# Kernel tuning notes

Measured on AMD Instinct MI355X. Metric: run time of the kernel, lower is better.

Reference implementation:

```python
import jax, jax.numpy as jnp
import numpy as np

B, N, E = 64, 512, 8192          # graphs, nodes per graph, edges per graph
F_IN, H, C = 128, 128, 10        # in features, hidden, classes
K1, K2 = 256, 128                # dense pool cluster counts: ceil(.5*N), ceil(.5*K1)
EPS = 1e-15


def setup_inputs():
    key = jax.random.key(0)
    keys = jax.random.split(key, 32)
    it = iter(keys)
    def w(shape, fan_in):
        return jax.random.normal(next(it), shape, jnp.float32) / np.sqrt(fan_in)
    x = jax.random.normal(next(it), (B * N, F_IN), jnp.float32)
    src_l = jax.random.randint(next(it), (B, E), 0, N)
    dst_l = jax.random.randint(next(it), (B, E), 0, N)
    off = (jnp.arange(B) * N)[:, None]
    src = (src_l + off).reshape(-1).astype(jnp.int32)
    dst = (dst_l + off).reshape(-1).astype(jnp.int32)
    return dict(
        x=x, src=src, dst=dst,
        conv0_wr=w((F_IN, H), F_IN), conv0_wroot=w((F_IN, H), F_IN), conv0_b=jnp.zeros((H,), jnp.float32),
        sconv2_wr=w((H, H), H), sconv2_wroot=w((H, H), H), sconv2_b=jnp.zeros((H,), jnp.float32),
        sconv3_wr=w((H, H), H), sconv3_wroot=w((H, H), H), sconv3_b=jnp.zeros((H,), jnp.float32),
        sage1_wr=w((H, H), H), sage1_wroot=w((H, H), H), sage1_b=jnp.zeros((H,), jnp.float32),
        sage2_wr=w((H, H), H), sage2_wroot=w((H, H), H), sage2_b=jnp.zeros((H,), jnp.float32),
        pool0_w=w((H, K1), H), pool0_b=jnp.zeros((K1,), jnp.float32),
        pool1_w=w((H, K2), H), pool1_b=jnp.zeros((K2,), jnp.float32),
        p1=w((H,), H), p2=w((H,), H), p3=w((H,), H),
        lin1_1_w=w((2 * H, H), 2 * H), lin1_1_b=jnp.zeros((H,), jnp.float32),
        lin1_w=w((H, H), H), lin1_b=jnp.zeros((H,), jnp.float32),
        lin2_w=w((2 * H, C), 2 * H), lin2_b=jnp.zeros((C,), jnp.float32),
    )


def _graph_conv(x, src, dst, emask, wr, wroot, b, n):
    # PyG GraphConv: lin_rel(sum_j x_j) + lin_root(x_i); invalid edges masked to 0.
    msg = x[src] * emask[:, None]
    agg = jax.ops.segment_sum(msg, dst, num_segments=n)
    return agg @ wr + x @ wroot + b


def _topk_pool(x, score_w, src, dst, emask, n_per_graph, k):
    # TopK pooling (MPoolS): score = x.w/||w||, keep top ratio*n per graph, gate by tanh(score).
    score = x @ score_w / (jnp.linalg.norm(score_w) + 1e-16)
    idx = jax.lax.top_k(score.reshape(B, n_per_graph), k)[1]
    perm = (idx + (jnp.arange(B) * n_per_graph)[:, None]).reshape(-1)
    new_x = x[perm] * jnp.tanh(score[perm])[:, None]
    new_id = jnp.full((B * n_per_graph,), -1, jnp.int32).at[perm].set(
        jnp.arange(B * k, dtype=jnp.int32))
    ns, nd = new_id[src], new_id[dst]
    valid = (ns >= 0) & (nd >= 0) & (emask > 0)
    return new_x, jnp.where(valid, ns, 0), jnp.where(valid, nd, 0), valid.astype(x.dtype)


def _readout(x, k):
    # gmp || gap per graph (nodes are contiguous, k per graph)
    xr = x.reshape(B, k, -1)
    return jnp.concatenate([xr.max(axis=1), xr.mean(axis=1)], axis=-1)


def _dense_sage(x, adj, wr, wroot, b):
    agg = (adj @ x) / jnp.clip(adj.sum(-1, keepdims=True), 1.0, None)
    return agg @ wr + x @ wroot + b


def _dense_mincut_pool(x, adj, s):
    s = jax.nn.softmax(s, axis=-1)
    k = s.shape[-1]
    out = jnp.einsum('bnk,bnf->bkf', s, x)
    out_adj = jnp.einsum('bnk,bnm,bml->bkl', s, adj, s)
    mincut_num = jnp.trace(out_adj, axis1=-2, axis2=-1)
    deg = adj.sum(-1)
    mincut_den = jnp.einsum('bn,bnk,bnk->b', deg, s, s)
    mc = -jnp.mean(mincut_num / (mincut_den + EPS))
    ss = jnp.einsum('bnk,bnl->bkl', s, s)
    ss_n = jnp.linalg.norm(ss, axis=(1, 2), keepdims=True)
    eye = jnp.eye(k, dtype=x.dtype)
    o = jnp.mean(jnp.linalg.norm(ss / (ss_n + EPS) - eye / jnp.sqrt(k), axis=(1, 2)))
    di = jnp.arange(k)
    out_adj = out_adj.at[:, di, di].set(0.0)
    dpool = jnp.sqrt(out_adj.sum(-1)) + EPS
    out_adj = out_adj / dpool[:, :, None] / dpool[:, None, :]
    return out, out_adj, mc, o


def _forward(x, src, dst, conv0_wr, conv0_wroot, conv0_b, sconv2_wr, sconv2_wroot, sconv2_b,
             sconv3_wr, sconv3_wroot, sconv3_b, sage1_wr, sage1_wroot, sage1_b,
             sage2_wr, sage2_wroot, sage2_b, pool0_w, pool0_b, pool1_w, pool1_b,
             p1, p2, p3, lin1_1_w, lin1_1_b, lin1_w, lin1_b, lin2_w, lin2_b):
    relu = jax.nn.relu
    e0 = jnp.ones((src.shape[0],), x.dtype)
    x0 = relu(_graph_conv(x, src, dst, e0, conv0_wr, conv0_wroot, conv0_b, B * N))
    # ---- sparse (MPoolS / top-k) branch, stage 1 ----
    sx, s1, d1, m1 = _topk_pool(x0, p1, src, dst, e0, N, N // 2)
    sx1 = _readout(sx, N // 2)
    # ---- dense (DiffPool-style) branch ----
    xd = x0.reshape(B, N, H)                               # to_dense_batch (full mask)
    g = src // N
    adj = jnp.zeros((B, N, N), x.dtype).at[g, src % N, dst % N].add(1.0)  # to_dense_adj
    s = xd @ pool0_w + pool0_b
    xd, adj, mc, o = _dense_mincut_pool(xd, adj, s)
    xd = relu(_dense_sage(xd, adj, sage1_wr, sage1_wroot, sage1_b))
    s = xd @ pool1_w + pool1_b
    xd, adj, mc2, o2 = _dense_mincut_pool(xd, adj, s)
    mc, o = mc + mc2, o + o2
    xd = _dense_sage(xd, adj, sage2_wr, sage2_wroot, sage2_b)
    xg = relu(xd.mean(axis=1) @ lin1_w + lin1_b)
    # ---- sparse branch, stages 2 and 3 ----
    sx = relu(_graph_conv(sx, s1, d1, m1, sconv2_wr, sconv2_wroot, sconv2_b, B * (N // 2)))
    sx, s2, d2, m2 = _topk_pool(sx, p2, s1, d1, m1, N // 2, N // 4)
    sx2 = _readout(sx, N // 4)
    sx = relu(_graph_conv(sx, s2, d2, m2, sconv3_wr, sconv3_wroot, sconv3_b, B * (N // 4)))
    sx, s3, d3, m3 = _topk_pool(sx, p3, s2, d2, m2, N // 4, N // 8)
    sx3 = _readout(sx, N // 8)
    sxr = relu((sx1 + sx2 + sx3) @ lin1_1_w + lin1_1_b)
    logits = jnp.concatenate([sxr, xg], axis=-1) @ lin2_w + lin2_b
    return logits, mc, o


def reference(x, src, dst, conv0_wr, conv0_wroot, conv0_b, sconv2_wr, sconv2_wroot, sconv2_b,
              sconv3_wr, sconv3_wroot, sconv3_b, sage1_wr, sage1_wroot, sage1_b,
              sage2_wr, sage2_wroot, sage2_b, pool0_w, pool0_b, pool1_w, pool1_b,
              p1, p2, p3, lin1_1_w, lin1_1_b, lin1_w, lin1_b, lin2_w, lin2_b):
    return _forward(x, src, dst, conv0_wr, conv0_wroot, conv0_b, sconv2_wr, sconv2_wroot,
                    sconv2_b, sconv3_wr, sconv3_wroot, sconv3_b, sage1_wr, sage1_wroot,
                    sage1_b, sage2_wr, sage2_wroot, sage2_b, pool0_w, pool0_b, pool1_w,
                    pool1_b, p1, p2, p3, lin1_1_w, lin1_1_b, lin1_w, lin1_b, lin2_w, lin2_b)
```

## Files before the change

### kernel.cpp

```cpp
#include <hip/hip_runtime.h>
#include <math.h>

#define NGRAPH 64
#define NE 524288
#define EPG 8192
#define TSZ 2560

typedef short s16x8 __attribute__((ext_vector_type(8)));
typedef float f32x4 __attribute__((ext_vector_type(4)));

__device__ inline unsigned short f2bf(float f) {
    unsigned int u = __float_as_uint(f);
    return (unsigned short)((u + 0x7FFFu + ((u >> 16) & 1u)) >> 16);
}
__device__ inline float bf2f(unsigned short h) {
    return __uint_as_float((unsigned int)h << 16);
}
__device__ inline unsigned int f2pk(float v) {
    unsigned short h = f2bf(v);
    return (unsigned int)h | ((unsigned int)f2bf(v - bf2f(h)) << 16);
}

__global__ void edge_count2(const int* __restrict__ keyA, int* __restrict__ cntA,
                            const int* __restrict__ keyB, int* __restrict__ cntB) {
    int e = blockIdx.x * 256 + threadIdx.x;
    if (e >= NE) return;
    if (blockIdx.y == 0) atomicAdd(&cntA[keyA[e]], 1);
    else                 atomicAdd(&cntB[keyB[e]], 1);
}

__device__ inline void scan_body(const int* __restrict__ counts, int* __restrict__ offs,
                                 int* __restrict__ cursor, int nPerGraph,
                                 float* __restrict__ degOut, int* s) {
    const int g = blockIdx.x, t = threadIdx.x;
    int v = (t < nPerGraph) ? counts[g * nPerGraph + t] : 0;
    s[t] = v; __syncthreads();
    for (int d = 1; d < 512; d <<= 1) {
        int u = (t >= d) ? s[t - d] : 0;
        __syncthreads();
        s[t] += u;
        __syncthreads();
    }
    if (t < nPerGraph) {
        int o = g * EPG + s[t] - v;
        offs[g * nPerGraph + t] = o;
        cursor[g * nPerGraph + t] = o;
        if (degOut) degOut[g * nPerGraph + t] = (float)v;
    }
}

__global__ __launch_bounds__(512) void scan_offsets(const int* __restrict__ counts,
        int* __restrict__ offs, int* __restrict__ cursor, int nPerGraph,
        float* __restrict__ degOut) {
    __shared__ int s[512];
    scan_body(counts, offs, cursor, nPerGraph, degOut, s);
}

__global__ __launch_bounds__(512) void scan_offsets2(
        const int* __restrict__ cA, int* __restrict__ oA, int* __restrict__ uA,
        const int* __restrict__ cB, int* __restrict__ oB, int* __restrict__ uB,
        int nPerGraph, float* __restrict__ degB) {
    __shared__ int s[512];
    if (blockIdx.y == 0) scan_body(cA, oA, uA, nPerGraph, nullptr, s);
    else                 scan_body(cB, oB, uB, nPerGraph, degB, s);
}

__global__ void edge_fill(const int* __restrict__ key, const int* __restrict__ payload,
                          const float* __restrict__ mask, int* __restrict__ cursor,
                          int* __restrict__ elist) {
    int e = blockIdx.x * 256 + threadIdx.x;
    if (e < NE && (!mask || mask[e] > 0.f)) {
        int p = atomicAdd(&cursor[key[e]], 1);
        elist[p] = payload[e];
    }
}

__global__ void edge_fill2(const int* __restrict__ kA, const int* __restrict__ pA,
                           int* __restrict__ uA, int* __restrict__ eA,
                           const int* __restrict__ kB, const int* __restrict__ pB,
                           int* __restrict__ uB, int* __restrict__ eB) {
    int e = blockIdx.x * 256 + threadIdx.x;
    if (e >= NE) return;
    if (blockIdx.y == 0) { int p = atomicAdd(&uA[kA[e]], 1); eA[p] = pA[e]; }
    else                 { int p = atomicAdd(&uB[kB[e]], 1); eB[p] = pB[e]; }
}

__global__ __launch_bounds__(256) void gather_csr(
    const float* __restrict__ xfeat, int Fx,
    const int* __restrict__ offs, const int* __restrict__ cnts,
    const int* __restrict__ elist,
    float* __restrict__ out, unsigned int* __restrict__ opk,
    int totRows, int rowsPerGraph)
{
    const int gid = (blockIdx.x * 256 + threadIdx.x) >> 5;
    const int lane = threadIdx.x & 31;
    const int csh = (Fx == 256) ? 1 : 0;
    const int rid = gid >> csh;
    const int c0 = (gid & ((1 << csh) - 1)) << 7;
    if (rid >= totRows) return;
    const int row = (rid & 63) * rowsPerGraph + (rid >> 6);
    const int beg = offs[row];
    const int n = cnts[row];
    const long long co = (long long)c0 + (lane << 2);
    float4 acc = make_float4(0.f, 0.f, 0.f, 0.f);
    int j = 0;
    for (; j + 4 <= n; j += 4) {
        const int n0 = elist[beg + j], n1 = elist[beg + j + 1];
        const int n2 = elist[beg + j + 2], n3 = elist[beg + j + 3];
        const float4 v0 = *(const float4*)&xfeat[(long long)n0 * Fx + co];
        const float4 v1 = *(const float4*)&xfeat[(long long)n1 * Fx + co];
        const float4 v2 = *(const float4*)&xfeat[(long long)n2 * Fx + co];
        const float4 v3 = *(const float4*)&xfeat[(long long)n3 * Fx + co];
        acc.x += v0.x + v1.x + v2.x + v3.x;
        acc.y += v0.y + v1.y + v2.y + v3.y;
        acc.z += v0.z + v1.z + v2.z + v3.z;
        acc.w += v0.w + v1.w + v2.w + v3.w;
    }
    for (; j < n; ++j) {
        const float4 v = *(const float4*)&xfeat[(long long)elist[beg + j] * Fx + co];
        acc.x += v.x; acc.y += v.y; acc.z += v.z; acc.w += v.w;
    }
    if (opk) {
        uint4 pk;
        pk.x = f2pk(acc.x); pk.y = f2pk(acc.y); pk.z = f2pk(acc.z); pk.w = f2pk(acc.w);
        *(uint4*)&opk[(long long)row * Fx + co] = pk;
    } else {
        *(float4*)&out[(long long)row * Fx + co] = acc;
    }
}

struct WSpec {
    const float* w1; const float* w2; int K1; int K2; int Nn;
    unsigned short* oh; unsigned short* ol;
};

__global__ void wconv_all(WSpec s0, WSpec s1, WSpec s2, WSpec s3, WSpec s4, WSpec s5, WSpec s6) {
    WSpec s;
    switch (blockIdx.y) {
        case 0: s = s0; break; case 1: s = s1; break; case 2: s = s2; break;
        case 3: s = s3; break; case 4: s = s4; break; case 5: s = s5; break;
        default: s = s6; break;
    }
    int idx = blockIdx.x * 256 + threadIdx.x;
    int Kt = s.K1 + s.K2;
    if (idx >= s.Nn * Kt) return;
    int n = idx / Kt, k = idx - n * Kt;
    float v = (k < s.K1) ? s.w1[(long long)k * s.Nn + n] : s.w2[(long long)(k - s.K1) * s.Nn + n];
    unsigned short h = f2bf(v);
    s.oh[idx] = h;
    s.ol[idx] = f2bf(v - __uint_as_float((unsigned int)h << 16));
}

__device__ inline void stageN_split(const float* __restrict__ src, int ldk, int k0,
                                    short* lds, int tid, const float* __restrict__ rs, int m0) {
    const int r = tid >> 2, kq = (tid & 3) << 3;
    const float* p = src + (long long)r * ldk + k0 + kq;
    float v[8];
    *(float4*)v = *(const float4*)p;
    *(float4*)(v + 4) = *(const float4*)(p + 4);
    if (rs) { float s = rs[m0 + r]; for (int i = 0; i < 8; ++i) v[i] *= s; }
    s16x8 hv, lv;
    #pragma unroll
    for (int i = 0; i < 8; ++i) {
        unsigned short h = f2bf(v[i]);
        float hf = __uint_as_float((unsigned int)h << 16);
        hv[i] = (short)h;
        lv[i] = (short)f2bf(v[i] - hf);
    }
    *(s16x8*)(lds + r * 40 + kq) = hv;
    *(s16x8*)(lds + TSZ + r * 40 + kq) = lv;
}

__device__ inline void stageT_pk(const unsigned int* __restrict__ P,
                                 int ldm, int k0, int m0, short* lds, int tid) {
    const int kp = tid >> 4, mc = tid & 15;
    const int k = kp << 1;
    const unsigned int* p0 = P + (long long)(k0 + k) * ldm + m0 + mc;
    const unsigned int* p1 = p0 + ldm;
    #pragma unroll
    for (int i = 0; i < 4; ++i) {
        unsigned int e0 = p0[i << 4], e1 = p1[i << 4];
        const int o = (mc + (i << 4)) * 40 + k;
        *(unsigned int*)(lds + o) = (e0 & 0xffffu) | (e1 << 16);
        *(unsigned int*)(lds + o + TSZ) = (e0 >> 16) | (e1 & 0xffff0000u);
    }
}

__device__ inline void stageT_hi_pk(const unsigned int* __restrict__ P,
                                    int ldm, int k0, int m0, short* lds, int tid) {
    const int kp = tid >> 4, mc = tid & 15;
    const int k = kp << 1;
    const unsigned int* p0 = P + (long long)(k0 + k) * ldm + m0 + mc;
    const unsigned int* p1 = p0 + ldm;
    #pragma unroll
    for (int i = 0; i < 4; ++i) {
        unsigned int e0 = p0[i << 4], e1 = p1[i << 4];
        *(unsigned int*)(lds + (mc + (i << 4)) * 40 + k) = (e0 & 0xffffu) | (e1 << 16);
    }
}

__device__ inline void stageW_split(const unsigned short* __restrict__ wh,
                                    const unsigned short* __restrict__ wl, int ldk,
                                    int n0, int k0, short* lds, int tid) {
    const int r = tid >> 2, kq = (tid & 3) << 3;
    *(s16x8*)(lds + r * 40 + kq) = *(const s16x8*)(wh + (long long)(n0 + r) * ldk + k0 + kq);
    *(s16x8*)(lds + TSZ + r * 40 + kq) = *(const s16x8*)(wl + (long long)(n0 + r) * ldk + k0 + kq);
}

__device__ inline void mfma_split(const short* As, const short* Bs, int wm, int wn,
                                  int l15, int quad, f32x4 (&acc)[2][2]) {
    const int ko = quad << 3;
    s16x8 ah[2], al[2], bh[2], bl[2];
    #pragma unroll
    for (int i = 0; i < 2; ++i) {
        const int ra = (wm + (i << 4) + l15) * 40 + ko;
        const int rb = (wn + (i << 4) + l15) * 40 + ko;
        ah[i] = *(const s16x8*)&As[ra];
        al[i] = *(const s16x8*)&As[TSZ + ra];
        bh[i] = *(const s16x8*)&Bs[rb];
        bl[i] = *(const s16x8*)&Bs[TSZ + rb];
    }
    #pragma unroll
    for (int mi = 0; mi < 2; ++mi)
    #pragma unroll
    for (int ni = 0; ni < 2; ++ni) {
        f32x4 c = acc[mi][ni];
        c = __builtin_amdgcn_mfma_f32_16x16x32_bf16(ah[mi], bh[ni], c, 0, 0, 0);
        c = __builtin_amdgcn_mfma_f32_16x16x32_bf16(ah[mi], bl[ni], c, 0, 0, 0);
        c = __builtin_amdgcn_mfma_f32_16x16x32_bf16(al[mi], bh[ni], c, 0, 0, 0);
        acc[mi][ni] = c;
    }
}

__device__ inline void mfma_hi(const short* As, const short* Bs, int wm, int wn,
                               int l15, int quad, f32x4 (&acc)[2][2]) {
    const int ko = quad << 3;
    s16x8 ah[2], bh[2];
    #pragma unroll
    for (int i = 0; i < 2; ++i) {
        ah[i] = *(const s16x8*)&As[(wm + (i << 4) + l15) * 40 + ko];
        bh[i] = *(const s16x8*)&Bs[(wn + (i << 4) + l15) * 40 + ko];
    }
    #pragma unroll
    for (int mi = 0; mi < 2; ++mi)
    #pragma unroll
    for (int ni = 0; ni < 2; ++ni)
        acc[mi][ni] = __builtin_amdgcn_mfma_f32_16x16x32_bf16(ah[mi], bh[ni], acc[mi][ni], 0, 0, 0);
}

__global__ __launch_bounds__(256) void gemm_aw(
    const float* __restrict__ A1, int K1, const float* __restrict__ A2, int K2,
    const float* __restrict__ rscale,
    const unsigned short* __restrict__ Wh, const unsigned short* __restrict__ Wl,
    const float* __restrict__ bias, float* __restrict__ C,
    unsigned int* __restrict__ Cpk,
    int Nn, int doRelu)
{
    __shared__ short As[2 * TSZ], Bs[2 * TSZ];
    const int m0 = blockIdx.y << 6, n0 = blockIdx.x << 6;
    const int tid = threadIdx.x, lane = tid & 63, wv = tid >> 6;
    const int l15 = lane & 15, quad = lane >> 4;
    const int wm = (wv & 1) << 5, wn = (wv >> 1) << 5;
    f32x4 acc[2][2] = {};
    const int Kt = K1 + K2;
    for (int k0 = 0; k0 < Kt; k0 += 32) {
        if (k0 < K1) stageN_split(A1 + (long long)m0 * K1, K1, k0, As, tid, rscale, m0);
        else         stageN_split(A2 + (long long)m0 * K2, K2, k0 - K1, As, tid, nullptr, 0);
        stageW_split(Wh, Wl, Kt, n0, k0, Bs, tid);
        __syncthreads();
        mfma_split(As, Bs, wm, wn, l15, quad, acc);
        __syncthreads();
    }
    #pragma unroll
    for (int mi = 0; mi < 2; ++mi)
    #pragma unroll
    for (int ni = 0; ni < 2; ++ni) {
        const int col = n0 + wn + (ni << 4) + l15;
        const float bv = bias ? bias[col] : 0.f;
        #pragma unroll
        for (int r = 0; r < 4; ++r) {
            const int row = m0 + wm + (mi << 4) + (quad << 2) + r;
            float v = acc[mi][ni][r] + bv;
            if (doRelu) v = fmaxf(v, 0.f);
            C[(long long)row * Nn + col] = v;
            if (Cpk) Cpk[(long long)row * Nn + col] = f2pk(v);
        }
    }
}

__global__ __launch_bounds__(256) void gemm_tt(
    const unsigned int* __restrict__ Ap, const unsigned int* __restrict__ Bp,
    float* __restrict__ C, unsigned int* __restrict__ Cpk,
    float* __restrict__ fro,
    int Kd, int Mm, int Nn, int dual,
    long long sA, long long sB, long long sC)
{
    __shared__ short As[2 * TSZ], Bs[2 * TSZ], A2s[TSZ];
    __shared__ float redf[4];
    const int z = blockIdx.x;
    const unsigned int* Apz = Ap + (long long)z * sA;
    const unsigned int* Bpz = Bp + (long long)z * sB;
    const int m0 = blockIdx.y << 6, n0 = blockIdx.z << 6;
    const int tid = threadIdx.x, lane = tid & 63, wv = tid >> 6;
    const int l15 = lane & 15, quad = lane >> 4;
    const int wm = (wv & 1) << 5, wn = (wv >> 1) << 5;
    const int fw = dual ? ((m0 < n0) ? 2 : ((m0 == n0) ? 1 : 0)) : 0;
    f32x4 acc[2][2] = {};
    f32x4 accA[2][2] = {};
    for (int k0 = 0; k0 < Kd; k0 += 32) {
        stageT_pk(Apz, Mm, k0, m0, As, tid);
        stageT_pk(Bpz, Nn, k0, n0, Bs, tid);
        if (fw) stageT_hi_pk(Apz, Mm, k0, n0, A2s, tid);
        __syncthreads();
        mfma_split(As, Bs, wm, wn, l15, quad, acc);
        if (fw) mfma_hi(As, A2s, wm, wn, l15, quad, accA);
        __syncthreads();
    }
    float* Cp = C ? C + (long long)z * sC : nullptr;
    unsigned int* Ckp = Cpk ? Cpk + (long long)z * sC : nullptr;
    #pragma unroll
    for (int mi = 0; mi < 2; ++mi)
    #pragma unroll
    for (int ni = 0; ni < 2; ++ni) {
        const int col = n0 + wn + (ni << 4) + l15;
        #pragma unroll
        for (int r = 0; r < 4; ++r) {
            const int row = m0 + wm + (mi << 4) + (quad << 2) + r;
            const float v = acc[mi][ni][r];
            if (Cp) Cp[(long long)row * Nn + col] = v;
            if (Ckp) Ckp[(long long)row * Nn + col] = f2pk(v);
        }
    }
    if (fw) {
        float s = 0.f;
        #pragma unroll
        for (int mi = 0; mi < 2; ++mi)
        #pragma unroll
        for (int ni = 0; ni < 2; ++ni)
        #pragma unroll
        for (int r = 0; r < 4; ++r) s += accA[mi][ni][r] * accA[mi][ni][r];
        s *= (float)fw;
        for (int off = 32; off; off >>= 1) s += __shfl_xor(s, off);
        if (lane == 0) redf[wv] = s;
        __syncthreads();
        if (tid == 0) atomicAdd(&fro[z], redf[0] + redf[1] + redf[2] + redf[3]);
    }
}

__global__ __launch_bounds__(256) void gemm_nt(
    const unsigned short* __restrict__ Ah, const unsigned short* __restrict__ Al,
    const unsigned int* __restrict__ Bp,
    float* __restrict__ C, unsigned int* __restrict__ Cpk,
    int Kd, int Nn, long long sA, long long sB, long long sC)
{
    __shared__ short As[2 * TSZ], Bs[2 * TSZ];
    const int z = blockIdx.x;
    const int m0 = blockIdx.y << 6, n0 = blockIdx.z << 6;
    const unsigned short* Aph = Ah + (long long)z * sA;
    const unsigned short* Apl = Al + (long long)z * sA;
    const unsigned int* Bpz = Bp + (long long)z * sB;
    const int tid = threadIdx.x, lane = tid & 63, wv = tid >> 6;
    const int l15 = lane & 15, quad = lane >> 4;
    const int wm = (wv & 1) << 5, wn = (wv >> 1) << 5;
    f32x4 acc[2][2] = {};
    for (int k0 = 0; k0 < Kd; k0 += 32) {
        stageW_split(Aph, Apl, Kd, m0, k0, As, tid);
        stageT_pk(Bpz, Nn, k0, n0, Bs, tid);
        __syncthreads();
        mfma_split(As, Bs, wm, wn, l15, quad, acc);
        __syncthreads();
    }
    #pragma unroll
    for (int mi = 0; mi < 2; ++mi)
    #pragma unroll
    for (int ni = 0; ni < 2; ++ni) {
        const int col = n0 + wn + (ni << 4) + l15;
        #pragma unroll
        for (int r = 0; r < 4; ++r) {
            const int row = m0 + wm + (mi << 4) + (quad << 2) + r;
            const float v = acc[mi][ni][r];
            if (C) C[(long long)z * sC + (long long)row * Nn + col] = v;
            if (Cpk) Cpk[(long long)z * sC + (long long)row * Nn + col] = f2pk(v);
        }
    }
}

__global__ __launch_bounds__(256) void softmax_rows_wave(
    float* __restrict__ sm, int L,
    const float* __restrict__ deg,
    float* __restrict__ rowq2, float* __restrict__ rowdq2, int totRows,
    unsigned int* __restrict__ opk)
{
    const int wid = (blockIdx.x * 256 + threadIdx.x) >> 6;
    const int lane = threadIdx.x & 63;
    if (wid >= totRows) return;
    float* rowp = sm + (long long)wid * L;
    const int nv = L >> 6;
    float v[4];
    if (nv == 4) {
        float4 t = *(const float4*)&rowp[lane << 2];
        v[0] = t.x; v[1] = t.y; v[2] = t.z; v[3] = t.w;
    } else {
        float2 t = *(const float2*)&rowp[lane << 1];
        v[0] = t.x; v[1] = t.y;
    }
    float mx = v[0];
    for (int i = 1; i < nv; ++i) mx = fmaxf(mx, v[i]);
    for (int off = 32; off; off >>= 1) mx = fmaxf(mx, __shfl_xor(mx, off));
    float s = 0.f;
    for (int i = 0; i < nv; ++i) { v[i] = expf(v[i] - mx); s += v[i]; }
    for (int off = 32; off; off >>= 1) s += __shfl_xor(s, off);
    const float inv = 1.f / s;
    float q2 = 0.f;
    for (int i = 0; i < nv; ++i) { float p = v[i] * inv; v[i] = p; q2 += p * p; }
    if (nv == 4) *(float4*)&rowp[lane << 2] = make_float4(v[0], v[1], v[2], v[3]);
    else         *(float2*)&rowp[lane << 1] = make_float2(v[0], v[1]);
    const long long rb = (long long)wid * L;
    if (nv == 4) {
        uint4 pk;
        pk.x = f2pk(v[0]); pk.y = f2pk(v[1]); pk.z = f2pk(v[2]); pk.w = f2pk(v[3]);
        *(uint4*)&opk[rb + (lane << 2)] = pk;
    } else {
        uint2 pk;
        pk.x = f2pk(v[0]); pk.y = f2pk(v[1]);
        *(uint2*)&opk[rb + (lane << 1)] = pk;
    }
    for (int off = 32; off; off >>= 1) q2 += __shfl_xor(q2, off);
    if (lane == 0) { rowq2[wid] = q2; rowdq2[wid] = deg[wid] * q2; }
}

__global__ __launch_bounds__(256) void zdiag_rowsum_wave(
    float* __restrict__ adj, int K, float* __restrict__ dpool,
    float* __restrict__ rowdiag, int totRows)
{
    const int wid = (blockIdx.x * 256 + threadIdx.x) >> 6;
    const int lane = threadIdx.x & 63;
    if (wid >= totRows) return;
    const int b = wid / K;
    const int dcol = wid - b * K;
    float* rowp = adj + (long long)wid * K;
    const int nv = K >> 6;
    float s = 0.f, dval = 0.f;
    for (int q = 0; q < nv; ++q) {
        int c = lane + (q << 6);
        float v = rowp[c];
        if (c == dcol) { dval = v; rowp[c] = 0.f; v = 0.f; }
        s += v;
    }
    for (int off = 32; off; off >>= 1) s += __shfl_xor(s, off);
    if (lane == (dcol & 63)) rowdiag[wid] = dval;
    if (lane == 0) dpool[wid] = sqrtf(s) + 1e-15f;
}

__global__ __launch_bounds__(256) void norm_adj_wave(
    const float* __restrict__ adj, int K, const float* __restrict__ dpool,
    float* __restrict__ rowsum, float* __restrict__ rscale,
    unsigned short* __restrict__ oh, unsigned short* __restrict__ ol, int totRows)
{
    const int wid = (blockIdx.x * 256 + threadIdx.x) >> 6;
    const int lane = threadIdx.x & 63;
    if (wid >= totRows) return;
    const int b = wid / K;
    const float* rowp = adj + (long long)wid * K;
    const float inv_r = 1.f / dpool[wid];
    const int nv = K >> 6;
    float s = 0.f;
    for (int q = 0; q < nv; ++q) {
        int c = lane + (q << 6);
        float v = rowp[c] * inv_r / dpool[b * K + c];
        s += v;
        unsigned short h = f2bf(v);
        oh[(long long)wid * K + c] = h;
        ol[(long long)wid * K + c] = f2bf(v - bf2f(h));
    }
    for (int off = 32; off; off >>= 1) s += __shfl_xor(s, off);
    if (lane == 0) { rowsum[wid] = s; rscale[wid] = 1.f / fmaxf(s, 1.f); }
}

__global__ __launch_bounds__(256) void reduce2_pergraph(
    const float* __restrict__ a, const float* __restrict__ b, int rowsPerGraph,
    float* __restrict__ outA, float* __restrict__ outB)
{
    __shared__ float redA[4], redB[4];
    const int g = blockIdx.x, t = threadIdx.x;
    float sa = 0.f, sb = 0.f;
    for (int i = t; i < rowsPerGraph; i += 256) {
        sa += a[g * rowsPerGraph + i];
        if (b) sb += b[g * rowsPerGraph + i];
    }
    for (int off = 32; off; off >>= 1) { sa += __shfl_xor(sa, off); sb += __shfl_xor(sb, off); }
    const int wv = t >> 6;
    if ((t & 63) == 0) { redA[wv] = sa; redB[wv] = sb; }
    __syncthreads();
    if (t == 0) {
        outA[g] = redA[0] + redA[1] + redA[2] + redA[3];
        if (outB) outB[g] = redB[0] + redB[1] + redB[2] + redB[3];
    }
}

// ... 117 lines not shown
}

__global__ void final_head(const float* __restrict__ sxsum, const float* __restrict__ w11,
                           const float* __restrict__ b11, const float* __restrict__ xg,
                           const float* __restrict__ w2, const float* __restrict__ b2,
                           const float* __restrict__ accs, float* __restrict__ out) {
    __shared__ float sin_[256];
    __shared__ float cat[256];
    __shared__ float rm[2], ro[2];
    int b = blockIdx.x, t = threadIdx.x;
    if (b == 0) {
        int wvi = t >> 6, lane = t & 63;
        const float* acc = accs + wvi * 256;
        float sqrtk = wvi ? sqrtf(128.f) : 16.f;
        float numv = acc[lane], denv = acc[64 + lane], trv = acc[128 + lane], frov = acc[192 + lane];
        float mcb = numv / (denv + 1e-15f);
        float ssn = sqrtf(frov) + 1e-15f;
        float ob = sqrtf(fmaxf(frov / (ssn * ssn) - 2.f * trv / (ssn * sqrtk) + 1.f, 0.f));
        for (int off = 32; off; off >>= 1) { mcb += __shfl_down(mcb, off); ob += __shfl_down(ob, off); }
        if (lane == 0) { rm[wvi] = mcb; ro[wvi] = ob; }
        __syncthreads();
        if (t == 0) {
            out[640] = -(rm[0] + rm[1]) / 64.f;
            out[641] = (ro[0] + ro[1]) / 64.f;
        }
    }
    sin_[t] = sxsum[b * 256 + t];
    sin_[t + 128] = sxsum[b * 256 + 128 + t];
    __syncthreads();
    float acc = b11[t];
    for (int i = 0; i < 256; i++) acc += sin_[i] * w11[i * 128 + t];
    cat[t] = fmaxf(acc, 0.f);
    cat[128 + t] = xg[b * 128 + t];
    __syncthreads();
    if (t < 10) {
        float a = b2[t];
        for (int i = 0; i < 256; i++) a += cat[i] * w2[i * 10 + t];
        out[b * 10 + t] = a;
    }
}

extern "C" void kernel_launch(void* const* d_in, const int* in_sizes, int n_in,
                              void* d_out, int out_size, void* d_ws, size_t ws_size,
                              hipStream_t stream) {
    const float* x         = (const float*)d_in[0];
    const int*   src       = (const int*)d_in[1];
    const int*   dst       = (const int*)d_in[2];
    const float* conv0_wr  = (const float*)d_in[3];
    const float* conv0_wrt = (const float*)d_in[4];
    const float* conv0_b   = (const float*)d_in[5];
    const float* sc2_wr    = (const float*)d_in[6];
    const float* sc2_wrt   = (const float*)d_in[7];
    const float* sc2_b     = (const float*)d_in[8];
    const float* sc3_wr    = (const float*)d_in[9];
    const float* sc3_wrt   = (const float*)d_in[10];
    const float* sc3_b     = (const float*)d_in[11];
    const float* sg1_wr    = (const float*)d_in[12];
    const float* sg1_wrt   = (const float*)d_in[13];
    const float* sg1_b     = (const float*)d_in[14];
    const float* sg2_wr    = (const float*)d_in[15];
    const float* sg2_wrt   = (const float*)d_in[16];
    const float* sg2_b     = (const float*)d_in[17];
    const float* pool0_w   = (const float*)d_in[18];
    const float* pool0_b   = (const float*)d_in[19];
    const float* pool1_w   = (const float*)d_in[20];
    const float* pool1_b   = (const float*)d_in[21];
    const float* p1        = (const float*)d_in[22];
    const float* p2        = (const float*)d_in[23];
    const float* p3        = (const float*)d_in[24];
    const float* l11_w     = (const float*)d_in[25];
    const float* l11_b     = (const float*)d_in[26];
    const float* l1_w      = (const float*)d_in[27];
    const float* l1_b      = (const float*)d_in[28];
    const float* l2_w      = (const float*)d_in[29];
    const float* l2_b      = (const float*)d_in[30];
    float* out = (float*)d_out;

    char* w = (char*)d_ws;
    const unsigned long long MBy = 1ull << 20;
    float* x0    = (float*)(w + 0);
    float* BIG1  = (float*)(w + 16 * MBy);
    float* BIG2  = (float*)(w + 48 * MBy);
    float* agg   = (float*)(w + 80 * MBy);
    float* outx1 = (float*)(w + 96 * MBy);
    float* adj1  = (float*)(w + 104 * MBy);
    int*   s1    = (int*)(w + 120 * MBy);
    int*   d1    = (int*)(w + 122 * MBy);
    float* m1    = (float*)(w + 124 * MBy);
    int*   s2e   = (int*)(w + 126 * MBy);
    int*   d2e   = (int*)(w + 128 * MBy);
    float* m2e   = (float*)(w + 130 * MBy);
    char*  misc  = w + 132 * MBy;
    float* score = (float*)(misc);
    int*   sel   = (int*)(misc + 128 * 1024);
    float* gate  = (float*)(misc + 192 * 1024);
    int*   newid = (int*)(misc + 256 * 1024);
    float* deg   = (float*)(misc + 384 * 1024);
    float* dpool = (float*)(misc + 512 * 1024);
    float* rowsum2 = (float*)(misc + 576 * 1024);
    float* rscale2 = (float*)(misc + 640 * 1024);
    float* dpool2  = (float*)(misc + 704 * 1024);
    float* rowsum3 = (float*)(misc + 736 * 1024);
    float* rscale3 = (float*)(misc + 768 * 1024);
    float* accs    = (float*)(misc + 800 * 1024);
    float* sxsum   = (float*)(misc + 900 * 1024);
    float* xg      = (float*)(misc + 964 * 1024);

    unsigned short* wt_sg1h   = (unsigned short*)(misc + 1024 * 1024);
    unsigned short* wt_sg1l   = wt_sg1h + 32768;
    unsigned short* wt_sg2h   = wt_sg1l + 32768;
    unsigned short* wt_sg2l   = wt_sg2h + 32768;
    unsigned short* wt_pool0h = wt_sg2l + 32768;
    unsigned short* wt_pool0l = wt_pool0h + 32768;
    unsigned short* wt_pool1h = wt_pool0l + 32768;
    unsigned short* wt_pool1l = wt_pool1h + 32768;
    unsigned short* wt_c0h    = wt_pool1l + 32768;
    unsigned short* wt_c0l    = wt_c0h + 32768;
    unsigned short* wt_sc2h   = wt_c0l + 32768;
    unsigned short* wt_sc2l   = wt_sc2h + 32768;
    unsigned short* wt_sc3h   = wt_sc2l + 32768;
    unsigned short* wt_sc3l   = wt_sc3h + 32768;

    float* pmax = (float*)(misc + 2048 * 1024);
    float* psum = pmax + 32768;

    float* rowq2  = score;
    float* rowdq2 = (float*)newid;
    float* rowdiag = (float*)sel;

    float* s_sm  = BIG1;
    unsigned int* Tbp = (unsigned int*)BIG2;
    float* xd1   = BIG2;
    float* AX    = BIG2 + 2 * 1024 * 1024;
    float* s2sm  = BIG2 + 4 * 1024 * 1024;
    unsigned int* T2p = (unsigned int*)((char*)BIG2 + 24 * MBy);
    float* outx2 = BIG1;
    float* adj2b = BIG1 + 1024 * 1024;
    float* xd2   = BIG1 + 2 * 1024 * 1024;
    float* sxA   = BIG1 + 3 * 1024 * 1024;
    float* sxE   = BIG1 + 5 * 1024 * 1024;
    float* sxB   = x0;
    float* sxC   = x0 + 2 * 1024 * 1024;
    float* sxD   = x0 + 3 * 1024 * 1024;

    unsigned int* s_smp = (unsigned int*)(w + 136 * MBy);
    unsigned int* x0p   = (unsigned int*)(w + 168 * MBy);
    unsigned int* ox1p  = (unsigned int*)(w + 184 * MBy);
    unsigned int* xd1p  = (unsigned int*)(w + 192 * MBy);
    unsigned int* s2p   = (unsigned int*)(w + 200 * MBy);
    unsigned int* ox2p  = (unsigned int*)(w + 208 * MBy);
    unsigned short* a1h = (unsigned short*)(w + 212 * MBy);
    unsigned short* a1l = (unsigned short*)(w + 220 * MBy);
    unsigned short* a2h = (unsigned short*)(w + 228 * MBy);
    unsigned short* a2l = (unsigned short*)(w + 230 * MBy);

    char* adjc = (char*)adj1;
    int* elA  = (int*)(adjc + 0);
    int* elB  = (int*)(adjc + 2 * MBy);
    int* cntA = (int*)(adjc + 4 * MBy);
    int* cntB = (int*)(adjc + 4 * MBy + 128 * 1024);
    int* offA = (int*)(adjc + 4 * MBy + 256 * 1024);
    int* curA = (int*)(adjc + 4 * MBy + 384 * 1024);
    int* offB = (int*)(adjc + 4 * MBy + 512 * 1024);
    int* curB = (int*)(adjc + 4 * MBy + 640 * 1024);
    char* aggc = (char*)agg;
    int* elC  = (int*)(aggc + 8 * MBy);
    int* elD  = (int*)(aggc + 10 * MBy);
    int* cntC = (int*)(aggc + 12 * MBy);
    int* offC = (int*)(aggc + 12 * MBy + 256 * 1024);
    int* curC = (int*)(aggc + 12 * MBy + 512 * 1024);
    int* cntD = (int*)(aggc + 13 * MBy);
    int* offD = (int*)(aggc + 13 * MBy + 256 * 1024);
    int* curD = (int*)(aggc + 13 * MBy + 512 * 1024);

    hipMemsetAsync(accs, 0, 520 * sizeof(float), stream);
    hipMemsetAsync(sxsum, 0, 16384 * sizeof(float), stream);
    hipMemsetAsync(cntA, 0, 65536 * sizeof(int), stream);

    {
        WSpec a{sg1_wr, sg1_wrt, 128, 128, 128, wt_sg1h, wt_sg1l};
        WSpec b{sg2_wr, sg2_wrt, 128, 128, 128, wt_sg2h, wt_sg2l};
        WSpec c{pool0_w, nullptr, 128, 0, 256, wt_pool0h, wt_pool0l};
        WSpec d{pool1_w, nullptr, 128, 0, 128, wt_pool1h, wt_pool1l};
        WSpec e{conv0_wr, conv0_wrt, 128, 128, 128, wt_c0h, wt_c0l};
        WSpec f{sc2_wr, sc2_wrt, 128, 128, 128, wt_sc2h, wt_sc2l};
        WSpec g{sc3_wr, sc3_wrt, 128, 128, 128, wt_sc3h, wt_sc3l};
        wconv_all<<<dim3(128, 7), 256, 0, stream>>>(a, b, c, d, e, f, g);
    }

    edge_count2<<<dim3(2048, 2), 256, 0, stream>>>(dst, cntA, src, cntB);
    scan_offsets2<<<dim3(64, 2), 512, 0, stream>>>(cntA, offA, curA, cntB, offB, curB, 512, deg);
    edge_fill2<<<dim3(2048, 2), 256, 0, stream>>>(dst, src, curA, elA, src, dst, curB, elB);

    gather_csr<<<4096, 256, 0, stream>>>(x, 128, offA, cntA, elA, agg, nullptr, 32768, 512);
    gemm_aw<<<dim3(2, 512), 256, 0, stream>>>(agg, 128, x, 128, nullptr, wt_c0h, wt_c0l,
        conv0_b, x0, x0p, 128, 1);

    gemm_aw<<<dim3(4, 512), 256, 0, stream>>>(x0, 128, nullptr, 0, nullptr, wt_pool0h, wt_pool0l,
        pool0_b, s_sm, nullptr, 256, 0);
    softmax_rows_wave<<<8192, 256, 0, stream>>>(s_sm, 256, deg, rowq2, rowdq2, 32768, s_smp);
    reduce2_pergraph<<<64, 256, 0, stream>>>(rowq2, rowdq2, 512, accs + 128, accs + 64);
    gather_csr<<<8192, 256, 0, stream>>>(s_sm, 256, offB, cntB, elB, nullptr, Tbp, 32768, 512);
    gemm_tt<<<dim3(64, 4, 2), 256, 0, stream>>>(s_smp, x0p, outx1, ox1p,
        nullptr, 512, 256, 128, 0, 512 * 256, 512 * 128, 256 * 128);
    gemm_tt<<<dim3(64, 4, 4), 256, 0, stream>>>(s_smp, Tbp, adj1, nullptr,
        accs + 192, 512, 256, 256, 1, 512 * 256, 512 * 256, 256 * 256);
    zdiag_rowsum_wave<<<4096, 256, 0, stream>>>(adj1, 256, dpool, rowdiag, 16384);
    reduce2_pergraph<<<64, 256, 0, stream>>>(rowdiag, nullptr, 256, accs + 0, nullptr);
    norm_adj_wave<<<4096, 256, 0, stream>>>(adj1, 256, dpool, rowsum2, rscale2, a1h, a1l, 16384);
    gemm_nt<<<dim3(64, 4, 2), 256, 0, stream>>>(a1h, a1l, ox1p, AX, nullptr,
        256, 128, 256 * 256, 256 * 128, 256 * 128);
    gemm_aw<<<dim3(2, 256), 256, 0, stream>>>(AX, 128, outx1, 128, rscale2, wt_sg1h, wt_sg1l,
        sg1_b, xd1, xd1p, 128, 1);
    gemm_aw<<<dim3(2, 256), 256, 0, stream>>>(xd1, 128, nullptr, 0, nullptr, wt_pool1h, wt_pool1l,
        pool1_b, s2sm, nullptr, 128, 0);
    softmax_rows_wave<<<4096, 256, 0, stream>>>(s2sm, 128, rowsum2, rowq2, rowdq2, 16384, s2p);
    reduce2_pergraph<<<64, 256, 0, stream>>>(rowq2, rowdq2, 256, accs + 384, accs + 320);
    gemm_nt<<<dim3(64, 4, 2), 256, 0, stream>>>(a1h, a1l, s2p, nullptr, T2p,
        256, 128, 256 * 256, 256 * 128, 256 * 128);
    gemm_tt<<<dim3(64, 2, 2), 256, 0, stream>>>(s2p, xd1p, outx2, ox2p,
        nullptr, 256, 128, 128, 0, 256 * 128, 256 * 128, 128 * 128);
    gemm_tt<<<dim3(64, 2, 2), 256, 0, stream>>>(s2p, T2p, adj2b, nullptr,
        accs + 448, 256, 128, 128, 1, 256 * 128, 256 * 128, 128 * 128);
    zdiag_rowsum_wave<<<2048, 256, 0, stream>>>(adj2b, 128, dpool2, rowdiag, 8192);
    reduce2_pergraph<<<64, 256, 0, stream>>>(rowdiag, nullptr, 128, accs + 256, nullptr);
    norm_adj_wave<<<2048, 256, 0, stream>>>(adj2b, 128, dpool2, rowsum3, rscale3, a2h, a2l, 8192);
    gemm_nt<<<dim3(64, 2, 2), 256, 0, stream>>>(a2h, a2l, ox2p, AX, nullptr,
        128, 128, 128 * 128, 128 * 128, 128 * 128);
    gemm_aw<<<dim3(2, 128), 256, 0, stream>>>(AX, 128, outx2, 128, rscale3, wt_sg2h, wt_sg2l,
        sg2_b, xd2, nullptr, 128, 0);
    mean_lin<<<64, 128, 0, stream>>>(xd2, l1_w, l1_b, xg, 128);

    topk_kernel<<<64, 512, 0, stream>>>(x0, p1, 512, 256, newid, sel, gate);
    gather_gate<<<2048, 256, 0, stream>>>(x0, sel, gate, sxA, 16384);
    hipMemsetAsync(cntC, 0, 16384 * sizeof(int), stream);
    remap_edges_count<<<2048, 256, 0, stream>>>(src, dst, nullptr, newid, s1, d1, m1, cntC);
    readout_part<<<dim3(64, 4), 128, 0, stream>>>(sxA, 256, pmax, psum);
    readout_comb<<<64, 128, 0, stream>>>(pmax, psum, 256, sxsum);
    scan_offsets<<<64, 512, 0, stream>>>(cntC, offC, curC, 256, nullptr);
    edge_fill<<<2048, 256, 0, stream>>>(d1, s1, m1, curC, elC);
    gather_csr<<<2048, 256, 0, stream>>>(sxA, 128, offC, cntC, elC, agg, nullptr, 16384, 256);
    gemm_aw<<<dim3(2, 256), 256, 0, stream>>>(agg, 128, sxA, 128, nullptr, wt_sc2h, wt_sc2l,
        sc2_b, sxB, nullptr, 128, 1);
    topk_kernel<<<64, 512, 0, stream>>>(sxB, p2, 256, 128, newid, sel, gate);
    gather_gate<<<1024, 256, 0, stream>>>(sxB, sel, gate, sxC, 8192);
    hipMemsetAsync(cntD, 0, 8192 * sizeof(int), stream);
    remap_edges_count<<<2048, 256, 0, stream>>>(s1, d1, m1, newid, s2e, d2e, m2e, cntD);
    readout_part<<<dim3(64, 4), 128, 0, stream>>>(sxC, 128, pmax, psum);
    readout_comb<<<64, 128, 0, stream>>>(pmax, psum, 128, sxsum);
    scan_offsets<<<64, 512, 0, stream>>>(cntD, offD, curD, 128, nullptr);
    edge_fill<<<2048, 256, 0, stream>>>(d2e, s2e, m2e, curD, elD);
    gather_csr<<<1024, 256, 0, stream>>>(sxC, 128, offD, cntD, elD, agg, nullptr, 8192, 128);
    gemm_aw<<<dim3(2, 128), 256, 0, stream>>>(agg, 128, sxC, 128, nullptr, wt_sc3h, wt_sc3l,
        sc3_b, sxD, nullptr, 128, 1);
    topk_kernel<<<64, 512, 0, stream>>>(sxD, p3, 128, 64, newid, sel, gate);
    gather_gate<<<512, 256, 0, stream>>>(sxD, sel, gate, sxE, 4096);
    readout_part<<<dim3(64, 4), 128, 0, stream>>>(sxE, 64, pmax, psum);
    readout_comb<<<64, 128, 0, stream>>>(pmax, psum, 64, sxsum);

    final_head<<<64, 128, 0, stream>>>(sxsum, l11_w, l11_b, xg, l2_w, l2_b, accs, out);
}
```

Measured before the change: 665.8 us.

## Pass packed bf16 hi/lo intermediates between kernels instead of fp32

Intermediate activations (aggregations, AX products, pooled features) are now written and read as packed hi/lo bf16 pairs, so the GEMM staging only reshuffles bits and no longer splits fp32 values. The row-scale multiply moves from gemm_aw staging into the gemm_nt epilogue. Redundant fp32 stores (softmax write-back, outx1/xd1 and AX in fp32) are removed. Memory traffic stays the same per element, but conversion work and several full-tensor writes go away. The hi+lo reconstruction in the gather adds a little ALU work and changes rounding slightly.

```diff
diff --git a/kernel.cpp b/kernel.cpp
--- a/kernel.cpp
+++ b/kernel.cpp
@@ -19,6 +19,9 @@
 __device__ inline unsigned int f2pk(float v) {
     unsigned short h = f2bf(v);
     return (unsigned int)h | ((unsigned int)f2bf(v - bf2f(h)) << 16);
+}
+__device__ inline float pk2f(unsigned int u) {
+    return __uint_as_float(u << 16) + __uint_as_float(u & 0xffff0000u);
 }
 
 __global__ void edge_count2(const int* __restrict__ keyA, int* __restrict__ cntA,
@@ -85,11 +88,18 @@
     else                 { int p = atomicAdd(&uB[kB[e]], 1); eB[p] = pB[e]; }
 }
 
+__device__ inline void addpk(float4& acc, uint4 u) {
+    acc.x += __uint_as_float(u.x << 16) + __uint_as_float(u.x & 0xffff0000u);
+    acc.y += __uint_as_float(u.y << 16) + __uint_as_float(u.y & 0xffff0000u);
+    acc.z += __uint_as_float(u.z << 16) + __uint_as_float(u.z & 0xffff0000u);
+    acc.w += __uint_as_float(u.w << 16) + __uint_as_float(u.w & 0xffff0000u);
+}
+
 __global__ __launch_bounds__(256) void gather_csr(
-    const float* __restrict__ xfeat, int Fx,
+    const float* __restrict__ xf, const unsigned int* __restrict__ xp, int Fx,
     const int* __restrict__ offs, const int* __restrict__ cnts,
     const int* __restrict__ elist,
-    float* __restrict__ out, unsigned int* __restrict__ opk,
+    unsigned int* __restrict__ opk,
     int totRows, int rowsPerGraph)
 {
     const int gid = (blockIdx.x * 256 + threadIdx.x) >> 5;
@@ -104,29 +114,39 @@
     const long long co = (long long)c0 + (lane << 2);
     float4 acc = make_float4(0.f, 0.f, 0.f, 0.f);
     int j = 0;
-    for (; j + 4 <= n; j += 4) {
-        const int n0 = elist[beg + j], n1 = elist[beg + j + 1];
-        const int n2 = elist[beg + j + 2], n3 = elist[beg + j + 3];
-        const float4 v0 = *(const float4*)&xfeat[(long long)n0 * Fx + co];
-        const float4 v1 = *(const float4*)&xfeat[(long long)n1 * Fx + co];
-        const float4 v2 = *(const float4*)&xfeat[(long long)n2 * Fx + co];
-        const float4 v3 = *(const float4*)&xfeat[(long long)n3 * Fx + co];
-        acc.x += v0.x + v1.x + v2.x + v3.x;
-        acc.y += v0.y + v1.y + v2.y + v3.y;
-        acc.z += v0.z + v1.z + v2.z + v3.z;
-        acc.w += v0.w + v1.w + v2.w + v3.w;
-    }
-    for (; j < n; ++j) {
-        const float4 v = *(const float4*)&xfeat[(long long)elist[beg + j] * Fx + co];
-        acc.x += v.x; acc.y += v.y; acc.z += v.z; acc.w += v.w;
-    }
-    if (opk) {
-        uint4 pk;
-        pk.x = f2pk(acc.x); pk.y = f2pk(acc.y); pk.z = f2pk(acc.z); pk.w = f2pk(acc.w);
-        *(uint4*)&opk[(long long)row * Fx + co] = pk;
+    if (xp) {
+        for (; j + 4 <= n; j += 4) {
+            const int n0 = elist[beg + j], n1 = elist[beg + j + 1];
+            const int n2 = elist[beg + j + 2], n3 = elist[beg + j + 3];
+            const uint4 u0 = *(const uint4*)&xp[(long long)n0 * Fx + co];
+            const uint4 u1 = *(const uint4*)&xp[(long long)n1 * Fx + co];
+            const uint4 u2 = *(const uint4*)&xp[(long long)n2 * Fx + co];
+            const uint4 u3 = *(const uint4*)&xp[(long long)n3 * Fx + co];
+            addpk(acc, u0); addpk(acc, u1); addpk(acc, u2); addpk(acc, u3);
+        }
+        for (; j < n; ++j)
+            addpk(acc, *(const uint4*)&xp[(long long)elist[beg + j] * Fx + co]);
     } else {
-        *(float4*)&out[(long long)row * Fx + co] = acc;
-    }
+        for (; j + 4 <= n; j += 4) {
+            const int n0 = elist[beg + j], n1 = elist[beg + j + 1];
+            const int n2 = elist[beg + j + 2], n3 = elist[beg + j + 3];
+            const float4 v0 = *(const float4*)&xf[(long long)n0 * Fx + co];
+            const float4 v1 = *(const float4*)&xf[(long long)n1 * Fx + co];
+            const float4 v2 = *(const float4*)&xf[(long long)n2 * Fx + co];
+            const float4 v3 = *(const float4*)&xf[(long long)n3 * Fx + co];
+            acc.x += v0.x + v1.x + v2.x + v3.x;
+            acc.y += v0.y + v1.y + v2.y + v3.y;
+            acc.z += v0.z + v1.z + v2.z + v3.z;
+            acc.w += v0.w + v1.w + v2.w + v3.w;
+        }
+        for (; j < n; ++j) {
+            const float4 v = *(const float4*)&xf[(long long)elist[beg + j] * Fx + co];
+            acc.x += v.x; acc.y += v.y; acc.z += v.z; acc.w += v.w;
+        }
+    }
+    uint4 pk;
+    pk.x = f2pk(acc.x); pk.y = f2pk(acc.y); pk.z = f2pk(acc.z); pk.w = f2pk(acc.w);
+    *(uint4*)&opk[(long long)row * Fx + co] = pk;
 }
 
 struct WSpec {
@@ -152,13 +172,12 @@
 }
 
 __device__ inline void stageN_split(const float* __restrict__ src, int ldk, int k0,
-                                    short* lds, int tid, const float* __restrict__ rs, int m0) {
+                                    short* lds, int tid) {
     const int r = tid >> 2, kq = (tid & 3) << 3;
     const float* p = src + (long long)r * ldk + k0 + kq;
     float v[8];
     *(float4*)v = *(const float4*)p;
     *(float4*)(v + 4) = *(const float4*)(p + 4);
-    if (rs) { float s = rs[m0 + r]; for (int i = 0; i < 8; ++i) v[i] *= s; }
     s16x8 hv, lv;
     #pragma unroll
     for (int i = 0; i < 8; ++i) {
@@ -169,6 +188,25 @@
     }
     *(s16x8*)(lds + r * 40 + kq) = hv;
     *(s16x8*)(lds + TSZ + r * 40 + kq) = lv;
+}
+
+__device__ inline void stageN_pk(const unsigned int* __restrict__ src, int ldk, int k0,
+                                 short* lds, int tid) {
+    const int r = tid >> 2, kq = (tid & 3) << 3;
+    const unsigned int* p = src + (long long)r * ldk + k0 + kq;
+    uint4 a = *(const uint4*)p;
+    uint4 b = *(const uint4*)(p + 4);
+    uint4 hw, lw;
+    hw.x = (a.x & 0xffffu) | (a.y << 16);
+    hw.y = (a.z & 0xffffu) | (a.w << 16);
+    hw.z = (b.x & 0xffffu) | (b.y << 16);
+    hw.w = (b.z & 0xffffu) | (b.w << 16);
+    lw.x = (a.x >> 16) | (a.y & 0xffff0000u);
+    lw.y = (a.z >> 16) | (a.w & 0xffff0000u);
+    lw.z = (b.x >> 16) | (b.y & 0xffff0000u);
+    lw.w = (b.z >> 16) | (b.w & 0xffff0000u);
+    *(uint4*)(lds + r * 40 + kq) = hw;
+    *(uint4*)(lds + TSZ + r * 40 + kq) = lw;
 }
 
 __device__ inline void stageT_pk(const unsigned int* __restrict__ P,
@@ -249,8 +287,8 @@
 }
 
 __global__ __launch_bounds__(256) void gemm_aw(
-    const float* __restrict__ A1, int K1, const float* __restrict__ A2, int K2,
-    const float* __restrict__ rscale,
+    const unsigned int* __restrict__ A1p, const float* __restrict__ A1f, int K1,
+    const unsigned int* __restrict__ A2p, const float* __restrict__ A2f, int K2,
     const unsigned short* __restrict__ Wh, const unsigned short* __restrict__ Wl,
     const float* __restrict__ bias, float* __restrict__ C,
     unsigned int* __restrict__ Cpk,
@@ -264,8 +302,13 @@
     f32x4 acc[2][2] = {};
     const int Kt = K1 + K2;
     for (int k0 = 0; k0 < Kt; k0 += 32) {
-        if (k0 < K1) stageN_split(A1 + (long long)m0 * K1, K1, k0, As, tid, rscale, m0);
-        else         stageN_split(A2 + (long long)m0 * K2, K2, k0 - K1, As, tid, nullptr, 0);
+        if (k0 < K1) {
+            if (A1p) stageN_pk(A1p + (long long)m0 * K1, K1, k0, As, tid);
+            else     stageN_split(A1f + (long long)m0 * K1, K1, k0, As, tid);
+        } else {
+            if (A2p) stageN_pk(A2p + (long long)m0 * K2, K2, k0 - K1, As, tid);
+            else     stageN_split(A2f + (long long)m0 * K2, K2, k0 - K1, As, tid);
+        }
         stageW_split(Wh, Wl, Kt, n0, k0, Bs, tid);
         __syncthreads();
         mfma_split(As, Bs, wm, wn, l15, quad, acc);
@@ -282,7 +325,7 @@
             const int row = m0 + wm + (mi << 4) + (quad << 2) + r;
             float v = acc[mi][ni][r] + bv;
             if (doRelu) v = fmaxf(v, 0.f);
-            C[(long long)row * Nn + col] = v;
+            if (C)   C[(long long)row * Nn + col] = v;
             if (Cpk) Cpk[(long long)row * Nn + col] = f2pk(v);
         }
     }
@@ -327,7 +370,7 @@
         for (int r = 0; r < 4; ++r) {
             const int row = m0 + wm + (mi << 4) + (quad << 2) + r;
             const float v = acc[mi][ni][r];
-            if (Cp) Cp[(long long)row * Nn + col] = v;
+            if (Cp)  Cp[(long long)row * Nn + col] = v;
             if (Ckp) Ckp[(long long)row * Nn + col] = f2pk(v);
         }
     }
@@ -351,6 +394,7 @@
     const unsigned short* __restrict__ Ah, const unsigned short* __restrict__ Al,
     const unsigned int* __restrict__ Bp,
     float* __restrict__ C, unsigned int* __restrict__ Cpk,
+    const float* __restrict__ rscale, int rsn,
     int Kd, int Nn, long long sA, long long sB, long long sC)
 {
     __shared__ short As[2 * TSZ], Bs[2 * TSZ];
@@ -378,15 +422,16 @@
         #pragma unroll
         for (int r = 0; r < 4; ++r) {
             const int row = m0 + wm + (mi << 4) + (quad << 2) + r;
-            const float v = acc[mi][ni][r];
-            if (C) C[(long long)z * sC + (long long)row * Nn + col] = v;
+            float v = acc[mi][ni][r];
+            if (rscale) v *= rscale[z * rsn + row];
+            if (C)   C[(long long)z * sC + (long long)row * Nn + col] = v;
             if (Cpk) Cpk[(long long)z * sC + (long long)row * Nn + col] = f2pk(v);
         }
     }
 }
 
 __global__ __launch_bounds__(256) void softmax_rows_wave(
-    float* __restrict__ sm, int L,
+    const float* __restrict__ sm, int L,
     const float* __restrict__ deg,
     float* __restrict__ rowq2, float* __restrict__ rowdq2, int totRows,
     unsigned int* __restrict__ opk)
@@ -394,7 +439,7 @@
     const int wid = (blockIdx.x * 256 + threadIdx.x) >> 6;
     const int lane = threadIdx.x & 63;
     if (wid >= totRows) return;
-    float* rowp = sm + (long long)wid * L;
+    const float* rowp = sm + (long long)wid * L;
     const int nv = L >> 6;
     float v[4];
     if (nv == 4) {
@@ -413,8 +458,6 @@
     const float inv = 1.f / s;
     float q2 = 0.f;
     for (int i = 0; i < nv; ++i) { float p = v[i] * inv; v[i] = p; q2 += p * p; }
-    if (nv == 4) *(float4*)&rowp[lane << 2] = make_float4(v[0], v[1], v[2], v[3]);
-    else         *(float2*)&rowp[lane << 1] = make_float2(v[0], v[1]);
     const long long rb = (long long)wid * L;
     if (nv == 4) {
         uint4 pk;
@@ -698,7 +741,6 @@
     float* BIG1  = (float*)(w + 16 * MBy);
     float* BIG2  = (float*)(w + 48 * MBy);
     float* agg   = (float*)(w + 80 * MBy);
-    float* outx1 = (float*)(w + 96 * MBy);
     float* adj1  = (float*)(w + 104 * MBy);
     int*   s1    = (int*)(w + 120 * MBy);
     int*   d1    = (int*)(w + 122 * MBy);
@@ -746,8 +788,6 @@
 
     float* s_sm  = BIG1;
     unsigned int* Tbp = (unsigned int*)BIG2;
-    float* xd1   = BIG2;
-    float* AX    = BIG2 + 2 * 1024 * 1024;
     float* s2sm  = BIG2 + 4 * 1024 * 1024;
     unsigned int* T2p = (unsigned int*)((char*)BIG2 + 24 * MBy);
     float* outx2 = BIG1;
@@ -769,6 +809,12 @@
     unsigned short* a1l = (unsigned short*)(w + 220 * MBy);
     unsigned short* a2h = (unsigned short*)(w + 228 * MBy);
     unsigned short* a2l = (unsigned short*)(w + 230 * MBy);
+    unsigned int* AXp   = (unsigned int*)(w + 232 * MBy);
+    unsigned int* AXp2  = (unsigned int*)(w + 240 * MBy);
+
+    unsigned int* aggp  = (unsigned int*)agg;
+    unsigned int* agg2p = (unsigned int*)agg;
+    unsigned int* agg3p = (unsigned int*)agg;
 
     char* adjc = (char*)adj1;
     int* elA  = (int*)(adjc + 0);
@@ -808,43 +854,43 @@
     scan_offsets2<<<dim3(64, 2), 512, 0, stream>>>(cntA, offA, curA, cntB, offB, curB, 512, deg);
     edge_fill2<<<dim3(2048, 2), 256, 0, stream>>>(dst, src, curA, elA, src, dst, curB, elB);
 
-    gather_csr<<<4096, 256, 0, stream>>>(x, 128, offA, cntA, elA, agg, nullptr, 32768, 512);
-    gemm_aw<<<dim3(2, 512), 256, 0, stream>>>(agg, 128, x, 128, nullptr, wt_c0h, wt_c0l,
-        conv0_b, x0, x0p, 128, 1);
-
-    gemm_aw<<<dim3(4, 512), 256, 0, stream>>>(x0, 128, nullptr, 0, nullptr, wt_pool0h, wt_pool0l,
-        pool0_b, s_sm, nullptr, 256, 0);
+    gather_csr<<<4096, 256, 0, stream>>>(x, nullptr, 128, offA, cntA, elA, aggp, 32768, 512);
+    gemm_aw<<<dim3(2, 512), 256, 0, stream>>>(aggp, nullptr, 128, nullptr, x, 128,
+        wt_c0h, wt_c0l, conv0_b, x0, x0p, 128, 1);
+
+    gemm_aw<<<dim3(4, 512), 256, 0, stream>>>(x0p, nullptr, 128, nullptr, nullptr, 0,
+        wt_pool0h, wt_pool0l, pool0_b, s_sm, nullptr, 256, 0);
     softmax_rows_wave<<<8192, 256, 0, stream>>>(s_sm, 256, deg, rowq2, rowdq2, 32768, s_smp);
     reduce2_pergraph<<<64, 256, 0, stream>>>(rowq2, rowdq2, 512, accs + 128, accs + 64);
-    gather_csr<<<8192, 256, 0, stream>>>(s_sm, 256, offB, cntB, elB, nullptr, Tbp, 32768, 512);
-    gemm_tt<<<dim3(64, 4, 2), 256, 0, stream>>>(s_smp, x0p, outx1, ox1p,
+    gather_csr<<<8192, 256, 0, stream>>>(nullptr, s_smp, 256, offB, cntB, elB, Tbp, 32768, 512);
+    gemm_tt<<<dim3(64, 4, 2), 256, 0, stream>>>(s_smp, x0p, nullptr, ox1p,
         nullptr, 512, 256, 128, 0, 512 * 256, 512 * 128, 256 * 128);
     gemm_tt<<<dim3(64, 4, 4), 256, 0, stream>>>(s_smp, Tbp, adj1, nullptr,
         accs + 192, 512, 256, 256, 1, 512 * 256, 512 * 256, 256 * 256);
     zdiag_rowsum_wave<<<4096, 256, 0, stream>>>(adj1, 256, dpool, rowdiag, 16384);
     reduce2_pergraph<<<64, 256, 0, stream>>>(rowdiag, nullptr, 256, accs + 0, nullptr);
     norm_adj_wave<<<4096, 256, 0, stream>>>(adj1, 256, dpool, rowsum2, rscale2, a1h, a1l, 16384);
-    gemm_nt<<<dim3(64, 4, 2), 256, 0, stream>>>(a1h, a1l, ox1p, AX, nullptr,
+    gemm_nt<<<dim3(64, 4, 2), 256, 0, stream>>>(a1h, a1l, ox1p, nullptr, AXp, rscale2, 256,
         256, 128, 256 * 256, 256 * 128, 256 * 128);
-    gemm_aw<<<dim3(2, 256), 256, 0, stream>>>(AX, 128, outx1, 128, rscale2, wt_sg1h, wt_sg1l,
-        sg1_b, xd1, xd1p, 128, 1);
-    gemm_aw<<<dim3(2, 256), 256, 0, stream>>>(xd1, 128, nullptr, 0, nullptr, wt_pool1h, wt_pool1l,
-        pool1_b, s2sm, nullptr, 128, 0);
+    gemm_aw<<<dim3(2, 256), 256, 0, stream>>>(AXp, nullptr, 128, ox1p, nullptr, 128,
+        wt_sg1h, wt_sg1l, sg1_b, nullptr, xd1p, 128, 1);
+    gemm_aw<<<dim3(2, 256), 256, 0, stream>>>(xd1p, nullptr, 128, nullptr, nullptr, 0,
+        wt_pool1h, wt_pool1l, pool1_b, s2sm, nullptr, 128, 0);
     softmax_rows_wave<<<4096, 256, 0, stream>>>(s2sm, 128, rowsum2, rowq2, rowdq2, 16384, s2p);
     reduce2_pergraph<<<64, 256, 0, stream>>>(rowq2, rowdq2, 256, accs + 384, accs + 320);
-    gemm_nt<<<dim3(64, 4, 2), 256, 0, stream>>>(a1h, a1l, s2p, nullptr, T2p,
+    gemm_nt<<<dim3(64, 4, 2), 256, 0, stream>>>(a1h, a1l, s2p, nullptr, T2p, nullptr, 0,
         256, 128, 256 * 256, 256 * 128, 256 * 128);
-    gemm_tt<<<dim3(64, 2, 2), 256, 0, stream>>>(s2p, xd1p, outx2, ox2p,
+    gemm_tt<<<dim3(64, 2, 2), 256, 0, stream>>>(s2p, xd1p, nullptr, ox2p,
         nullptr, 256, 128, 128, 0, 256 * 128, 256 * 128, 128 * 128);
     gemm_tt<<<dim3(64, 2, 2), 256, 0, stream>>>(s2p, T2p, adj2b, nullptr,
         accs + 448, 256, 128, 128, 1, 256 * 128, 256 * 128, 128 * 128);
     zdiag_rowsum_wave<<<2048, 256, 0, stream>>>(adj2b, 128, dpool2, rowdiag, 8192);
     reduce2_pergraph<<<64, 256, 0, stream>>>(rowdiag, nullptr, 128, accs + 256, nullptr);
     norm_adj_wave<<<2048, 256, 0, stream>>>(adj2b, 128, dpool2, rowsum3, rscale3, a2h, a2l, 8192);
-    gemm_nt<<<dim3(64, 2, 2), 256, 0, stream>>>(a2h, a2l, ox2p, AX, nullptr,
+    gemm_nt<<<dim3(64, 2, 2), 256, 0, stream>>>(a2h, a2l, ox2p, nullptr, AXp2, rscale3, 128,
         128, 128, 128 * 128, 128 * 128, 128 * 128);
-    gemm_aw<<<dim3(2, 128), 256, 0, stream>>>(AX, 128, outx2, 128, rscale3, wt_sg2h, wt_sg2l,
-        sg2_b, xd2, nullptr, 128, 0);
+    gemm_aw<<<dim3(2, 128), 256, 0, stream>>>(AXp2, nullptr, 128, ox2p, nullptr, 128,
+        wt_sg2h, wt_sg2l, sg2_b, xd2, nullptr, 128, 0);
     mean_lin<<<64, 128, 0, stream>>>(xd2, l1_w, l1_b, xg, 128);
 
     topk_kernel<<<64, 512, 0, stream>>>(x0, p1, 512, 256, newid, sel, gate);
@@ -855,9 +901,9 @@
     readout_comb<<<64, 128, 0, stream>>>(pmax, psum, 256, sxsum);
     scan_offsets<<<64, 512, 0, stream>>>(cntC, offC, curC, 256, nullptr);
     edge_fill<<<2048, 256, 0, stream>>>(d1, s1, m1, curC, elC);
-    gather_csr<<<2048, 256, 0, stream>>>(sxA, 128, offC, cntC, elC, agg, nullptr, 16384, 256);
-    gemm_aw<<<dim3(2, 256), 256, 0, stream>>>(agg, 128, sxA, 128, nullptr, wt_sc2h, wt_sc2l,
-        sc2_b, sxB, nullptr, 128, 1);
+    gather_csr<<<2048, 256, 0, stream>>>(sxA, nullptr, 128, offC, cntC, elC, agg2p, 16384, 256);
+    gemm_aw<<<dim3(2, 256), 256, 0, stream>>>(agg2p, nullptr, 128, nullptr, sxA, 128,
+        wt_sc2h, wt_sc2l, sc2_b, sxB, nullptr, 128, 1);
     topk_kernel<<<64, 512, 0, stream>>>(sxB, p2, 256, 128, newid, sel, gate);
     gather_gate<<<1024, 256, 0, stream>>>(sxB, sel, gate, sxC, 8192);
     hipMemsetAsync(cntD, 0, 8192 * sizeof(int), stream);
@@ -866,9 +912,9 @@
     readout_comb<<<64, 128, 0, stream>>>(pmax, psum, 128, sxsum);
     scan_offsets<<<64, 512, 0, stream>>>(cntD, offD, curD, 128, nullptr);
     edge_fill<<<2048, 256, 0, stream>>>(d2e, s2e, m2e, curD, elD);
-    gather_csr<<<1024, 256, 0, stream>>>(sxC, 128, offD, cntD, elD, agg, nullptr, 8192, 128);
-    gemm_aw<<<dim3(2, 128), 256, 0, stream>>>(agg, 128, sxC, 128, nullptr, wt_sc3h, wt_sc3l,
-        sc3_b, sxD, nullptr, 128, 1);
+    gather_csr<<<1024, 256, 0, stream>>>(sxC, nullptr, 128, offD, cntD, elD, agg3p, 8192, 128);
+    gemm_aw<<<dim3(2, 128), 256, 0, stream>>>(agg3p, nullptr, 128, nullptr, sxC, 128,
+        wt_sc3h, wt_sc3l, sc3_b, sxD, nullptr, 128, 1);
     topk_kernel<<<64, 512, 0, stream>>>(sxD, p3, 128, 64, newid, sel, gate);
     gather_gate<<<512, 256, 0, stream>>>(sxD, sel, gate, sxE, 4096);
     readout_part<<<dim3(64, 4), 128, 0, stream>>>(sxE, 64, pmax, psum);
```

Result: no change. 667.4 us (+0.2%).
